# Optimization experiments

Hardware: AMD Instinct MI355X
Metric: run time of the kernel (lower is better)

## Reference

```python
import jax, jax.numpy as jnp
import numpy as np

N = 20000; P = 3; L_LP = 10; L_NS = 20; D = 128; OUT = 2; E = 640000; V_LP = 5000; V_NS = 10000


def _gru(x, lengths, W_ih, W_hh, b_ih, b_hh):
    # x: [B, T, Din]; returns last valid hidden state per sequence (pack_padded semantics)
    T = x.shape[1]
    xp = jnp.einsum('btd,gd->btg', x, W_ih) + b_ih  # [B, T, 3H]
    h0 = jnp.zeros((x.shape[0], W_hh.shape[1]), x.dtype)

    def step(h, inp):
        xpt, t = inp
        hp = h @ W_hh.T + b_hh
        xr, xz, xn = jnp.split(xpt, 3, axis=-1)
        hr, hz, hn = jnp.split(hp, 3, axis=-1)
        r = jax.nn.sigmoid(xr + hr)
        z = jax.nn.sigmoid(xz + hz)
        nn_ = jnp.tanh(xn + r * hn)
        h_new = (1.0 - z) * nn_ + z * h
        h = jnp.where((t < lengths)[:, None], h_new, h)
        return h, None

    hT, _ = jax.lax.scan(step, h0, (jnp.swapaxes(xp, 0, 1), jnp.arange(T)))
    return hT


def _gcn(x, src, dst, w, W, b, n):
    # PyG GCNConv: add self-loops (weight 1), symmetric normalization by in-degree
    loops = jnp.arange(n)
    s = jnp.concatenate([src, loops])
    d = jnp.concatenate([dst, loops])
    ww = jnp.concatenate([w, jnp.ones((n,), w.dtype)])
    deg = jax.ops.segment_sum(ww, d, num_segments=n)
    dinv = jnp.where(deg > 0, 1.0 / jnp.sqrt(deg), 0.0)
    norm = dinv[s] * ww * dinv[d]
    xw = x @ W.T
    return jax.ops.segment_sum(norm[:, None] * xw[s], d, num_segments=n) + b


def _lnorm(x, g, b):
    m = jnp.mean(x, axis=-1, keepdims=True)
    v = jnp.var(x, axis=-1, keepdims=True)
    return (x - m) / jnp.sqrt(v + 1e-5) * g + b


def _forward(x_ref, x_def, x_pdt, edge_weight, lp_emb, ns_emb, lp_Wih, lp_Whh, lp_bih, lp_bhh, ns_Wih, ns_Whh, ns_bih, ns_bhh, lp_fc_W, lp_fc_b, all_fc_W, all_fc_b, conv1_W, conv1_b, conv2_W, conv2_b, conv3_W, conv3_b, ln1_g, ln1_b, ln2_g, ln2_b, mp1_W, mp1_b, mp2_W, mp2_b, idx_lp, x_lp_length, idx_ns, x_ns_length, edge_index):
    n = idx_ns.shape[0]
    # long-path GRU encodings, one GRU run per path slot (vmapped over P)
    xl = lp_emb[idx_lp]  # [N, P, L_LP, D]
    gru_lp = lambda seq, lens: _gru(seq, lens, lp_Wih, lp_Whh, lp_bih, lp_bhh)
    h_lp = jax.vmap(gru_lp, in_axes=(1, 1))(xl, x_lp_length)  # [P, N, D]
    # torch.cat(h_list).view(N, D*P): row-major reshape of [P, N, D]
    x_lp = h_lp.reshape(n, P * D) @ lp_fc_W.T + lp_fc_b
    # natural-sequence GRU encoding
    x_ns = _gru(ns_emb[idx_ns], x_ns_length, ns_Wih, ns_Whh, ns_bih, ns_bhh)  # [N, D]
    # torch.cat(dim=0).view(N, 5D): faithful row-major reshape of [5N, D]
    x = jnp.concatenate([x_pdt, x_ref, x_def, x_lp, x_ns], axis=0).reshape(n, 5 * D)
    x = x @ all_fc_W.T + all_fc_b
    src, dst = edge_index[0], edge_index[1]
    convs = [(conv1_W, conv1_b), (conv2_W, conv2_b), (conv3_W, conv3_b)]
    lns = [(ln1_g, ln1_b), (ln2_g, ln2_b)]
    emb = x
    for i in range(3):
        x = _gcn(x, src, dst, edge_weight, convs[i][0], convs[i][1], n)
        emb = x
        x = jax.nn.relu(x)
        # dropout p=0.25 omitted (eval mode)
        if i < 2:
            x = _lnorm(x, lns[i][0], lns[i][1])
    x = x @ mp1_W.T + mp1_b
    x = x @ mp2_W.T + mp2_b
    return emb, jax.nn.log_softmax(x, axis=1)


def setup_inputs() -> dict:
    ks = jax.random.split(jax.random.key(0), 40)
    f32 = jnp.float32
    nrm = lambda k, sh, s: jax.random.normal(k, sh, f32) * s
    inp = {}
    inp['idx_lp'] = jax.random.randint(ks[0], (N, P, L_LP), 0, V_LP)
    inp['x_lp_length'] = jax.random.randint(ks[1], (N, P), 1, L_LP + 1)
    inp['idx_ns'] = jax.random.randint(ks[2], (N, L_NS), 0, V_NS)
    inp['x_ns_length'] = jax.random.randint(ks[3], (N,), 1, L_NS + 1)
    inp['x_ref'] = nrm(ks[4], (N, D), 1.0)
    inp['x_def'] = nrm(ks[5], (N, D), 1.0)
    inp['x_pdt'] = nrm(ks[6], (N, D), 1.0)
    inp['edge_index'] = jax.random.randint(ks[7], (2, E), 0, N)
    inp['edge_weight'] = jax.random.uniform(ks[8], (E,), f32)
    inp['lp_emb'] = nrm(ks[9], (V_LP, D), 0.5)
    inp['ns_emb'] = nrm(ks[10], (V_NS, D), 0.5)
    s = 0.08
    inp['lp_Wih'] = nrm(ks[11], (3 * D, D), s)
    inp['lp_Whh'] = nrm(ks[12], (3 * D, D), s)
    inp['lp_bih'] = nrm(ks[13], (3 * D,), s)
    inp['lp_bhh'] = nrm(ks[14], (3 * D,), s)
    inp['ns_Wih'] = nrm(ks[15], (3 * D, D), s)
    inp['ns_Whh'] = nrm(ks[16], (3 * D, D), s)
    inp['ns_bih'] = nrm(ks[17], (3 * D,), s)
    inp['ns_bhh'] = nrm(ks[18], (3 * D,), s)
    inp['lp_fc_W'] = nrm(ks[19], (D, P * D), 0.05)
    inp['lp_fc_b'] = nrm(ks[20], (D,), 0.05)
    inp['all_fc_W'] = nrm(ks[21], (D, 5 * D), 0.05)
    inp['all_fc_b'] = nrm(ks[22], (D,), 0.05)
    inp['conv1_W'] = nrm(ks[23], (D, D), 0.08)
    inp['conv1_b'] = nrm(ks[24], (D,), 0.05)
    inp['conv2_W'] = nrm(ks[25], (D, D), 0.08)
    inp['conv2_b'] = nrm(ks[26], (D,), 0.05)
    inp['conv3_W'] = nrm(ks[27], (D, D), 0.08)
    inp['conv3_b'] = nrm(ks[28], (D,), 0.05)
    inp['ln1_g'] = jnp.ones((D,), f32)
    inp['ln1_b'] = jnp.zeros((D,), f32)
    inp['ln2_g'] = jnp.ones((D,), f32)
    inp['ln2_b'] = jnp.zeros((D,), f32)
    inp['mp1_W'] = nrm(ks[29], (D, D), 0.08)
    inp['mp1_b'] = nrm(ks[30], (D,), 0.05)
    inp['mp2_W'] = nrm(ks[31], (OUT, D), 0.08)
    inp['mp2_b'] = nrm(ks[32], (OUT,), 0.05)
    return inp


def reference(idx_lp, x_lp_length, idx_ns, x_ns_length, x_ref, x_def, x_pdt, edge_index, edge_weight, lp_emb, ns_emb, lp_Wih, lp_Whh, lp_bih, lp_bhh, ns_Wih, ns_Whh, ns_bih, ns_bhh, lp_fc_W, lp_fc_b, all_fc_W, all_fc_b, conv1_W, conv1_b, conv2_W, conv2_b, conv3_W, conv3_b, ln1_g, ln1_b, ln2_g, ln2_b, mp1_W, mp1_b, mp2_W, mp2_b):
    return _forward(x_ref, x_def, x_pdt, edge_weight, lp_emb, ns_emb, lp_Wih, lp_Whh, lp_bih, lp_bhh, ns_Wih, ns_Whh, ns_bih, ns_bhh, lp_fc_W, lp_fc_b, all_fc_W, all_fc_b, conv1_W, conv1_b, conv2_W, conv2_b, conv3_W, conv3_b, ln1_g, ln1_b, ln2_g, ln2_b, mp1_W, mp1_b, mp2_W, mp2_b, idx_lp, x_lp_length, idx_ns, x_ns_length, edge_index)
```

## Files before the change

### kernel.cpp

```cpp
#include <hip/hip_runtime.h>
#include <math.h>

typedef unsigned short u16;
typedef short bf16x4 __attribute__((ext_vector_type(4)));
typedef short bf16x8 __attribute__((ext_vector_type(8)));
typedef float f32x16 __attribute__((ext_vector_type(16)));

#define NN 20000
#define PP 3
#define TLP 10
#define TNS 20
#define DD 128
#define EE 640000

__device__ __forceinline__ float bf2f(u16 u) {
  union { unsigned u; float f; } v; v.u = ((unsigned)u) << 16; return v.f;
}
__device__ __forceinline__ u16 f2bf(float f) {
  union { float f; unsigned u; } v; v.f = f;
  unsigned r = v.u + 0x7fffu + ((v.u >> 16) & 1u);
  return (u16)(r >> 16);
}
__device__ __forceinline__ short f2bf_hw(float f) {
  __bf16 b = (__bf16)f;
  return (short)__builtin_bit_cast(unsigned short, b);
}
__device__ __forceinline__ float loadf(const void* p, size_t i, int isf) {
  return isf ? ((const float*)p)[i] : bf2f(((const u16*)p)[i]);
}
__device__ __forceinline__ float fex2(float x) { return __builtin_amdgcn_exp2f(x); }
__device__ __forceinline__ float frcp(float x) { return __builtin_amdgcn_rcpf(x); }
__device__ __forceinline__ unsigned cvtpk(float lo, float hi) {
  unsigned r; asm("v_cvt_pk_bf16_f32 %0, %1, %2" : "=v"(r) : "v"(lo), "v"(hi));
  return r;
}

__global__ void k_detect(const void* probe, int* flag, int* bins,
                         int* __restrict__ counts) {
  if (blockIdx.x > 0) {
    int i = (blockIdx.x - 1) * 256 + threadIdx.x;
    if (i < NN) counts[i] = 0;
    return;
  }
  __shared__ int any;
  if (threadIdx.x == 0) any = 0;
  __syncthreads();
  if (threadIdx.x < 128) bins[threadIdx.x] = 0;
  const u16* p = (const u16*)probe;
  int bad = 0;
  for (int i = threadIdx.x; i < 4096; i += 256) {
    int e = (p[2 * i] >> 7) & 0xFF;
    if (e >= 0x9F) bad = 1;
  }
  if (bad) atomicOr(&any, 1);
  __syncthreads();
  if (threadIdx.x == 0) flag[0] = any;
}

struct CvtJobs {
  const void* src[16];
  int off[16];
  int n[16];
};

struct CvtJobsB {
  const void* src[12];
  int off[12];
  int n[12];
  int thr[12];
  float scA[12];
  float scB[12];
};

__global__ void k_megacvt(CvtJobsB j, CvtJobs jf, u16* __restrict__ dst,
                          float* __restrict__ fdst,
                          const int* __restrict__ lensLP,
                          const int* __restrict__ lensNS,
                          int* __restrict__ bins,
                          const int* __restrict__ e_dst,
                          int* __restrict__ counts,
                          const void* __restrict__ w2raw,
                          const void* __restrict__ b1raw,
                          const void* __restrict__ b2raw,
                          const void* __restrict__ mp1raw,
                          float* __restrict__ Wc, const int* flag) {
  const int isf = flag[0];
  const int B_CVT = 12 * 64;
  const int B_F = B_CVT + 16;
  const int LEN_B = (PP * NN + 255) / 256;
  const int B_LEN = B_F + LEN_B;
  const int HIST_B = (EE + 255) / 256;
  const int B_HIST = B_LEN + HIST_B;
  const int bx = (int)blockIdx.x;
  const int tid = threadIdx.x;
  if (bx < B_CVT) {
    const int job = bx >> 6;
    if (job < 2 && !isf) return;
    const int chunk = bx & 63;
    const void* s = j.src[job];
    u16* d = dst + j.off[job];
    const int n = j.n[job];
    const int thr = j.thr[job];
    const float sA = j.scA[job], sB = j.scB[job];
    for (int i = chunk * 256 + tid; i < n; i += 64 * 256)
      d[i] = f2bf(loadf(s, i, isf) * (i < thr ? sA : sB));
    return;
  }
  if (bx < B_F) {
    const int job = bx - B_CVT;
    const void* s = jf.src[job];
    float* d = fdst + jf.off[job];
    const int n = jf.n[job];
    for (int i = tid; i < n; i += 256) d[i] = loadf(s, i, isf);
    return;
  }
  if (bx < B_LEN) {
    int sg = (bx - B_F) * 256 + tid;
    int lane = tid & 63;
    int binL = 0, binN = 0;
    if (sg < PP * NN) binL = lensLP[(sg % NN) * PP + sg / NN];
    if (sg < NN) binN = lensNS[sg];
    for (int b = 1; b <= TLP; ++b) {
      unsigned long long m = __ballot(binL == b);
      if (m) {
        int leader = (int)(__ffsll((long long)m) - 1);
        if (lane == leader) atomicAdd(&bins[b], (int)__popcll(m));
      }
    }
    for (int b = 1; b <= TNS; ++b) {
      unsigned long long m = __ballot(binN == b);
      if (m) {
        int leader = (int)(__ffsll((long long)m) - 1);
        if (lane == leader) atomicAdd(&bins[64 + b], (int)__popcll(m));
      }
    }
    return;
  }
  if (bx < B_HIST) {
    int e = (bx - B_LEN) * 256 + tid;
    if (e < EE) atomicAdd(&counts[e_dst[e]], 1);
    return;
  }
  const int o = tid >> 7, k = tid & 127;
  float acc = 0.f;
  for (int d2 = 0; d2 < 128; ++d2)
    acc += loadf(w2raw, o * 128 + d2, isf) * loadf(mp1raw, (size_t)d2 * 128 + k, isf);
  Wc[tid] = acc;
  if (tid < 2) {
    float bacc = loadf(b2raw, tid, isf);
    for (int d2 = 0; d2 < 128; ++d2)
      bacc += loadf(w2raw, tid * 128 + d2, isf) * loadf(b1raw, d2, isf);
    Wc[256 + tid] = bacc;
  }
}

__global__ void k_lenfillboth(const int* __restrict__ lensLP,
                              const int* __restrict__ lensNS,
                              int* __restrict__ bins,
                              int* __restrict__ permLP,
                              int* __restrict__ permNS) {
  int sg = blockIdx.x * 256 + threadIdx.x;
  int lane = threadIdx.x & 63;
  int binL = 0, binN = 0;
  if (sg < PP * NN) binL = lensLP[(sg % NN) * PP + sg / NN];
  if (sg < NN) binN = lensNS[sg];
  int baseL = 0;
  for (int b = 1; b <= TLP; ++b) {
    unsigned long long m = __ballot(binL == b);
    if (m) {
      int leader = (int)(__ffsll((long long)m) - 1);
      int base = 0;
      if (lane == leader) base = atomicAdd(&bins[32 + b], (int)__popcll(m));
      base = __shfl(base, leader);
      if (binL == b) {
        int rank = (int)__popcll(m & ((1ull << lane) - 1ull));
        permLP[baseL + base + rank] = sg;
      }
    }
    baseL += bins[b];
  }
  int baseN = 0;
  for (int b = 1; b <= TNS; ++b) {
    unsigned long long m = __ballot(binN == b);
    if (m) {
      int leader = (int)(__ffsll((long long)m) - 1);
      int base = 0;
      if (lane == leader) base = atomicAdd(&bins[96 + b], (int)__popcll(m));
      base = __shfl(base, leader);
      if (binN == b) {
        int rank = (int)__popcll(m & ((1ull << lane) - 1ull));
        permNS[baseN + base + rank] = sg;
      }
    }
    baseN += bins[64 + b];
  }
}

__global__ __launch_bounds__(512, 2) void k_gru5(
    const int* __restrict__ permLP, const int* __restrict__ permNS, int nbNS,
    const u16* __restrict__ embLPc, const u16* __restrict__ embNSc,
    const u16* __restrict__ embLPr, const u16* __restrict__ embNSr,
    const int* __restrict__ idxLP, const int* __restrict__ idxNS,
    const int* __restrict__ lenLP, const int* __restrict__ lenNS,
    const u16* __restrict__ WihLP, const u16* __restrict__ WhhLP,
    const u16* __restrict__ WihNS, const u16* __restrict__ WhhNS,
    const float* __restrict__ bihLP, const float* __restrict__ bhhLP,
    const float* __restrict__ bihNS, const float* __restrict__ bhhNS,
    u16* __restrict__ HoutLP, u16* __restrict__ HoutNS, int nbLP,
    const int* __restrict__ counts, int* __restrict__ startA,
    int* __restrict__ cursorE, const int* __restrict__ flag) {
  __shared__ u16 xp[2][3][128][36];
  __shared__ u16 Hbf2[2][32][132];
  __shared__ int ivs[TNS][32];
  __shared__ int rowv[32], outv[32], lenv_s[32];
  __shared__ int Tbs;

  const int tid = threadIdx.x;
  if (blockIdx.x == 0) {
    int* part = (int*)ivs;
    const int C = (NN + 255) / 256;
    if (tid < 256) {
      int base = tid * C;
      int s = 0;
      for (int k = 0; k < C; ++k) {
        int i2 = base + k;
        s += (i2 < NN) ? counts[i2] : 0;
      }
      part[tid] = s;
    }
    __syncthreads();
    if (tid == 0) {
      int acc = 0;
      for (int k = 0; k < 256; ++k) { int v = part[k]; part[k] = acc; acc += v; }
    }
    __syncthreads();
    if (tid < 256) {
      int run = part[tid];
      int base = tid * C;
      for (int k = 0; k < C; ++k) {
        int i2 = base + k;
        if (i2 < NN) {
          int c = counts[i2];
          startA[i2] = run;
          cursorE[i2] = run;
          run += c;
        }
      }
      if (tid == 255) startA[NN] = run;
    }
    return;
  }
  const int bid = blockIdx.x - 1;
  const int isf = flag[0];
  const int isNS = bid < nbNS;
  const int chunk = isNS ? (nbNS - 1 - bid) : (nbLP - 1 - (bid - nbNS));
  const int* perm = isNS ? (permNS + chunk * 32) : (permLP + chunk * 32);
  const u16* embbf = isNS ? (isf ? embNSc : embNSr) : (isf ? embLPc : embLPr);
  const int* idx = isNS ? idxNS : idxLP;
  const int* lens = isNS ? lenNS : lenLP;
  const u16* Wih = isNS ? WihNS : WihLP;
  const u16* Whh = isNS ? WhhNS : WhhLP;
  const float* bih = isNS ? bihNS : bihLP;
  const float* bhh = isNS ? bhhNS : bhhLP;
  u16* Hout = isNS ? HoutNS : HoutLP;
  const int T = isNS ? TNS : TLP;

  const int w = tid >> 6, lane = tid & 63;
  const int l31 = lane & 31, lh = lane >> 5;
  const int role = w >> 2;
  const int j = w & 3;
  const int d = 32 * j + l31;

  if (tid < 32) {
    int sg = perm[tid];
    int row = isNS ? sg : ((sg % NN) * PP + sg / NN);
    rowv[tid] = row;
    outv[tid] = sg;
    lenv_s[tid] = lens[row];
  }
  __syncthreads();
  if (tid == 0) {
    int m = 1;
    for (int k = 0; k < 32; ++k) m = max(m, lenv_s[k]);
    Tbs = m;
  }
  __syncthreads();
  const int Tb = Tbs;

  for (int z = tid; z < Tb * 32; z += 512) {
    int s = z & 31, t = z >> 5;
    ivs[t][s] = idx[(size_t)rowv[s] * T + t];
  }
  for (int z = tid; z < 2112; z += 512) ((unsigned*)Hbf2[0])[z] = 0u;

  bf16x8 wf[24];
  {
    const u16* Ws = role ? Whh : Wih;
#pragma unroll
    for (int g = 0; g < 3; ++g)
#pragma unroll
      for (int kb = 0; kb < 8; ++kb)
        wf[g * 8 + kb] =
            *(const bf16x8*)(Ws + (size_t)(128 * g + d) * 128 + kb * 16 + lh * 8);
  }
  const float SA = -1.44269504088896f;
  const float SN = -2.88539008177793f;
  float ib0, ib1, ib2;
  if (!role) {
    ib0 = SA * (bih[d] + bhh[d]);
    ib1 = SA * (bih[128 + d] + bhh[128 + d]);
    ib2 = SN * bih[256 + d];
  } else {
    ib0 = 0.f;
    ib1 = 0.f;
    ib2 = SN * bhh[256 + d];
  }

  __syncthreads();
  int lenr[16];
#pragma unroll
  for (int rg = 0; rg < 16; ++rg)
    lenr[rg] = lenv_s[(rg & 3) + 8 * (rg >> 2) + 4 * lh];

  float h[16];
#pragma unroll
  for (int rg = 0; rg < 16; ++rg) h[rg] = 0.f;

  for (int i = 0; i <= Tb; ++i) {
    if (!role) {
      if (i < Tb) {
        bf16x8 Xf[8];
        const u16* erow = embbf + (size_t)ivs[i][l31] * 128 + lh * 8;
#pragma unroll
        for (int kb = 0; kb < 8; ++kb) Xf[kb] = *(const bf16x8*)(erow + kb * 16);
        f32x16 a0 = (f32x16)(ib0), a1 = (f32x16)(ib1), a2 = (f32x16)(ib2);
#pragma unroll
        for (int kb = 0; kb < 8; ++kb) {
          a0 = __builtin_amdgcn_mfma_f32_32x32x16_bf16(Xf[kb], wf[kb], a0, 0, 0, 0);
          a1 = __builtin_amdgcn_mfma_f32_32x32x16_bf16(Xf[kb], wf[8 + kb], a1, 0, 0, 0);
          a2 = __builtin_amdgcn_mfma_f32_32x32x16_bf16(Xf[kb], wf[16 + kb], a2, 0, 0, 0);
        }
        const int sl = i & 1;
#pragma unroll
        for (int rq = 0; rq < 4; ++rq) {
          int mo = 8 * rq + 4 * lh;
          bf16x4 p0, p1, p2;
#pragma unroll
          for (int q = 0; q < 4; ++q) {
            p0[q] = f2bf_hw(a0[4 * rq + q]);
            p1[q] = f2bf_hw(a1[4 * rq + q]);
            p2[q] = f2bf_hw(a2[4 * rq + q]);
          }
          *(bf16x4*)(&xp[sl][0][d][mo]) = p0;
          *(bf16x4*)(&xp[sl][1][d][mo]) = p1;
          *(bf16x4*)(&xp[sl][2][d][mo]) = p2;
        }
      }
    } else {
      if (i >= 1) {
        const int rs = (i - 1) & 1, wsl = i & 1;
        bf16x8 Hf[8];
#pragma unroll
        for (int kb = 0; kb < 8; ++kb) {
          bf16x4 lo = *(const bf16x4*)(&Hbf2[rs][l31][16 * kb + 8 * lh]);
          bf16x4 hi = *(const bf16x4*)(&Hbf2[rs][l31][16 * kb + 8 * lh + 4]);
          Hf[kb] = __builtin_shufflevector(lo, hi, 0, 1, 2, 3, 4, 5, 6, 7);
        }
        f32x16 a0 = (f32x16)(ib0), a1 = (f32x16)(ib1), a2 = (f32x16)(ib2);
#pragma unroll
        for (int kb = 0; kb < 8; ++kb) {
          a0 = __builtin_amdgcn_mfma_f32_32x32x16_bf16(Hf[kb], wf[kb], a0, 0, 0, 0);
          a1 = __builtin_amdgcn_mfma_f32_32x32x16_bf16(Hf[kb], wf[8 + kb], a1, 0, 0, 0);
          a2 = __builtin_amdgcn_mfma_f32_32x32x16_bf16(Hf[kb], wf[16 + kb], a2, 0, 0, 0);
        }
        const int t = i - 1;
#pragma unroll
        for (int rq = 0; rq < 4; ++rq) {
          int mo = 8 * rq + 4 * lh;
          bf16x4 x0 = *(const bf16x4*)(&xp[rs][0][d][mo]);
          bf16x4 x1 = *(const bf16x4*)(&xp[rs][1][d][mo]);
          bf16x4 x2 = *(const bf16x4*)(&xp[rs][2][d][mo]);
          float hq[4];
#pragma unroll
          for (int q = 0; q < 4; ++q) {
            int rg = 4 * rq + q;
            float r = frcp(1.f + fex2(a0[rg] + bf2f((u16)x0[q])));
            float z = frcp(1.f + fex2(a1[rg] + bf2f((u16)x1[q])));
            float s = fmaf(r, a2[rg], bf2f((u16)x2[q]));
            float nn_ = fmaf(2.f, frcp(1.f + fex2(s)), -1.f);
            float hnew = fmaf(z, h[rg] - nn_, nn_);
            h[rg] = (t < lenr[rg]) ? hnew : h[rg];
            hq[q] = h[rg];
          }
          unsigned pa = cvtpk(hq[0], hq[1]);
          unsigned pb = cvtpk(hq[2], hq[3]);
          Hbf2[wsl][mo + 0][d] = (u16)pa;
          Hbf2[wsl][mo + 1][d] = (u16)(pa >> 16);
          Hbf2[wsl][mo + 2][d] = (u16)pb;
          Hbf2[wsl][mo + 3][d] = (u16)(pb >> 16);
        }
      }
    }
    __syncthreads();
  }

  if (role) {
#pragma unroll
    for (int rg = 0; rg < 16; ++rg) {
      int m = (rg & 3) + 8 * (rg >> 2) + 4 * lh;
      Hout[(size_t)outv[m] * 128 + d] = f2bf(h[rg]);
    }
  }
}

__global__ __launch_bounds__(128) void k_gemm_mfma(
    const void* __restrict__ A0, const void* __restrict__ A1,
    const void* __restrict__ A2, const u16* __restrict__ A3,
    const u16* __restrict__ A4, int mode, int K,
    const u16* __restrict__ W, const float* __restrict__ bias,
    void* __restrict__ Cout, int out_bf, int M, const int* __restrict__ flag,
    const int* __restrict__ esrc, const int* __restrict__ edst,
    const void* __restrict__ ew, int* __restrict__ cursor,
    int2* __restrict__ csr, const int* __restrict__ startT,
    float* __restrict__ dinvOut, int tailN, int tailMode, int gemmBlocks) {
  const int isf = flag[0];
  const int tid = threadIdx.x;
  if ((int)blockIdx.x >= gemmBlocks) {
    int i = ((int)blockIdx.x - gemmBlocks) * 128 + tid;
    if (i < tailN) {
      if (tailMode == 1) {
        int s = esrc[i];
        float wv = loadf(ew, i, isf);
        int p = atomicAdd(&cursor[edst[i]], 1);
        csr[p] = make_int2(s, __float_as_int(wv));
      } else {
        int a = startT[i], b = startT[i + 1];
        float sum = 1.f;
        for (int k = a; k < b; ++k) sum += __int_as_float(csr[k].y);
        dinvOut[i] = 1.f / sqrtf(sum);
      }
    }
    return;
  }
  const int w = tid >> 6, lane = tid & 63;
  const int l31 = lane & 31, lh = lane >> 5;
  const int w23 = w;
  const int mbase = blockIdx.x * 32;
  const int row = mbase + l31;
  const int rowc = row < M ? row : M - 1;

  f32x16 acc0 = (f32x16)(0.f), acc1 = (f32x16)(0.f);
  const int nk = K >> 4;
  for (int kb = 0; kb < nk; ++kb) {
    bf16x8 a;
    if (mode == 0) {
      a = *(const bf16x8*)((const u16*)A0 + (size_t)rowc * K + kb * 16 + lh * 8);
    } else {
      int r5 = 5 * rowc + (kb >> 3);
      int slot = r5 / NN;
      int inner = r5 - slot * NN;
      int koff = (kb & 7) * 16 + lh * 8;
      if (slot < 3) {
        const void* p = (slot == 0) ? A0 : (slot == 1) ? A1 : A2;
        if (isf) {
          const float* fp = (const float*)p + (size_t)inner * 128 + koff;
          float4 v0 = *(const float4*)fp;
          float4 v1 = *(const float4*)(fp + 4);
          a[0] = (short)f2bf(v0.x); a[1] = (short)f2bf(v0.y);
          a[2] = (short)f2bf(v0.z); a[3] = (short)f2bf(v0.w);
          a[4] = (short)f2bf(v1.x); a[5] = (short)f2bf(v1.y);
          a[6] = (short)f2bf(v1.z); a[7] = (short)f2bf(v1.w);
        } else {
          a = *(const bf16x8*)((const u16*)p + (size_t)inner * 128 + koff);
        }
      } else {
        const u16* p = (slot == 3) ? A3 : A4;
        a = *(const bf16x8*)(p + (size_t)inner * 128 + koff);
      }
    }
    const u16* wp = W + (size_t)(64 * w23 + l31) * K + kb * 16 + lh * 8;
    bf16x8 b0 = *(const bf16x8*)wp;
    bf16x8 b1 = *(const bf16x8*)(wp + (size_t)32 * K);
    acc0 = __builtin_amdgcn_mfma_f32_32x32x16_bf16(a, b0, acc0, 0, 0, 0);
    acc1 = __builtin_amdgcn_mfma_f32_32x32x16_bf16(a, b1, acc1, 0, 0, 0);
  }
  const int col0 = 64 * w23 + l31;
  const float bv0 = bias ? bias[col0] : 0.f;
  const float bv1 = bias ? bias[col0 + 32] : 0.f;
#pragma unroll
  for (int rg = 0; rg < 16; ++rg) {
    int m = (rg & 3) + 8 * (rg >> 2) + 4 * lh;
    int grow = mbase + m;
    if (grow < M) {
      float v0 = acc0[rg] + bv0, v1 = acc1[rg] + bv1;
      if (out_bf) {
        ((u16*)Cout)[(size_t)grow * 128 + col0] = f2bf(v0);
        ((u16*)Cout)[(size_t)grow * 128 + col0 + 32] = f2bf(v1);
      } else {
        ((float*)Cout)[(size_t)grow * 128 + col0] = v0;
        ((float*)Cout)[(size_t)grow * 128 + col0 + 32] = v1;
      }
    }
  }
}

__global__ __launch_bounds__(256) void k_gcn_gather(
    const int* __restrict__ start, const int2* __restrict__ csr,
    const float* __restrict__ dinv, const u16* __restrict__ xwbf,
    const float* __restrict__ bias, const float* __restrict__ g,
    const float* __restrict__ b, u16* __restrict__ out_bf,
    void* __restrict__ dout, const float* __restrict__ Wc,
    const int* __restrict__ flag, int mode) {
  int v = blockIdx.x * 4 + (threadIdx.x >> 6);
  int lane = threadIdx.x & 63;
  if (v >= NN) return;
  const int c0 = 2 * lane;
  float acc0 = 0.f, acc1 = 0.f;
  int i = start[v];
  const int i1 = start[v + 1];
  for (; i + 4 <= i1; i += 4) {
    int2 e0 = csr[i], e1 = csr[i + 1], e2 = csr[i + 2], e3 = csr[i + 3];
    unsigned p0 = *(const unsigned*)(xwbf + (size_t)e0.x * 128 + c0);
    unsigned p1 = *(const unsigned*)(xwbf + (size_t)e1.x * 128 + c0);
    unsigned p2 = *(const unsigned*)(xwbf + (size_t)e2.x * 128 + c0);
    unsigned p3 = *(const unsigned*)(xwbf + (size_t)e3.x * 128 + c0);
    float f0 = __int_as_float(e0.y) * dinv[e0.x];
    float f1 = __int_as_float(e1.y) * dinv[e1.x];
    float f2 = __int_as_float(e2.y) * dinv[e2.x];
    float f3 = __int_as_float(e3.y) * dinv[e3.x];
    acc0 += f0 * bf2f((u16)(p0 & 0xffff)) + f1 * bf2f((u16)(p1 & 0xffff)) +
            f2 * bf2f((u16)(p2 & 0xffff)) + f3 * bf2f((u16)(p3 & 0xffff));
    acc1 += f0 * bf2f((u16)(p0 >> 16)) + f1 * bf2f((u16)(p1 >> 16)) +
            f2 * bf2f((u16)(p2 >> 16)) + f3 * bf2f((u16)(p3 >> 16));
  }
  if (i + 2 <= i1) {
    int2 e0 = csr[i], e1 = csr[i + 1];
    unsigned p0 = *(const unsigned*)(xwbf + (size_t)e0.x * 128 + c0);
    unsigned p1 = *(const unsigned*)(xwbf + (size_t)e1.x * 128 + c0);
    float f0 = __int_as_float(e0.y) * dinv[e0.x];
    float f1 = __int_as_float(e1.y) * dinv[e1.x];
    acc0 += f0 * bf2f((u16)(p0 & 0xffff)) + f1 * bf2f((u16)(p1 & 0xffff));
    acc1 += f0 * bf2f((u16)(p0 >> 16)) + f1 * bf2f((u16)(p1 >> 16));
    i += 2;
  }
  if (i < i1) {
    int2 e = csr[i];
    float c = __int_as_float(e.y) * dinv[e.x];
    unsigned pv = *(const unsigned*)(xwbf + (size_t)e.x * 128 + c0);
    acc0 += c * bf2f((u16)(pv & 0xffff));
    acc1 += c * bf2f((u16)(pv >> 16));
  }
  float dv = dinv[v];
  unsigned sv = *(const unsigned*)(xwbf + (size_t)v * 128 + c0);
  float y0 = bias[c0] + dv * (dv * bf2f((u16)(sv & 0xffff)) + acc0);
  float y1 = bias[c0 + 1] + dv * (dv * bf2f((u16)(sv >> 16)) + acc1);
  if (mode == 1) {
    if (flag[0]) {
      *(float2*)((float*)dout + (size_t)v * 128 + c0) = make_float2(y0, y1);
    } else {
      unsigned pk = (unsigned)f2bf(y0) | ((unsigned)f2bf(y1) << 16);
      *(unsigned*)((u16*)dout + (size_t)v * 128 + c0) = pk;
    }
    float x0 = fmaxf(y0, 0.f), x1 = fmaxf(y1, 0.f);
    float p0 = x0 * Wc[c0] + x1 * Wc[c0 + 1];
    float p1 = x0 * Wc[128 + c0] + x1 * Wc[128 + c0 + 1];
#pragma unroll
    for (int off = 32; off; off >>= 1) {
      p0 += __shfl_xor(p0, off);
      p1 += __shfl_xor(p1, off);
    }
    if (lane == 0) {
      float v0 = p0 + Wc[256], v1 = p1 + Wc[257];
      float m = fmaxf(v0, v1);
      float ls = m + logf(__expf(v0 - m) + __expf(v1 - m));
      size_t base = (size_t)NN * 128 + (size_t)v * 2;
      if (flag[0]) {
        ((float*)dout)[base + 0] = v0 - ls;
        ((float*)dout)[base + 1] = v1 - ls;
      } else {
        unsigned pk = (unsigned)f2bf(v0 - ls) | ((unsigned)f2bf(v1 - ls) << 16);
        *(unsigned*)((u16*)dout + base) = pk;
      }
    }
  } else {
    float x0 = fmaxf(y0, 0.f), x1 = fmaxf(y1, 0.f);
    float s_ = x0 + x1;
#pragma unroll
    for (int off = 32; off; off >>= 1) s_ += __shfl_xor(s_, off);
    float mean = s_ * (1.f / 128.f);
    float e0 = x0 - mean, e1 = x1 - mean;
    float vv = e0 * e0 + e1 * e1;
#pragma unroll
    for (int off = 32; off; off >>= 1) vv += __shfl_xor(vv, off);
    float inv = 1.f / sqrtf(vv * (1.f / 128.f) + 1e-5f);
    unsigned pk = (unsigned)f2bf(e0 * inv * g[c0] + b[c0]) |
                  ((unsigned)f2bf(e1 * inv * g[c0 + 1] + b[c0 + 1]) << 16);
    *(unsigned*)(out_bf + (size_t)v * 128 + c0) = pk;
  }
}

extern "C" void kernel_launch(void* const* d_in, const int* in_sizes, int n_in,
                              void* d_out, int out_size, void* d_ws, size_t ws_size,
                              hipStream_t stream) {
  const int* idx_lp = (const int*)d_in[0];
  const int* len_lp = (const int*)d_in[1];
  const int* idx_ns = (const int*)d_in[2];
  const int* len_ns = (const int*)d_in[3];
  const void* x_ref = d_in[4];
  const void* x_def = d_in[5];
  const void* x_pdt = d_in[6];
  const int* eidx   = (const int*)d_in[7];
  const void* ew    = d_in[8];
  const void* lp_emb = d_in[9];
  const void* ns_emb = d_in[10];

  char* cur = (char*)d_ws;
  auto alloc = [&](size_t bytes, size_t align) -> void* {
    size_t a = ((size_t)cur + align - 1) & ~(align - 1);
    cur = (char*)(a + bytes);
    return (void*)a;
  };
  int* flag     = (int*)alloc(64, 64);
  float* smallW = (float*)alloc(3104 * 4, 16);
  float* f_Wc   = (float*)alloc(260 * 4, 16);
  float* f_dinv = (float*)alloc(NN * 4, 16);
  int* counts   = (int*)alloc(NN * 4, 16);
  int* startA   = (int*)alloc((NN + 1) * 4, 16);
  int* cursorE  = (int*)alloc(NN * 4, 16);
  int* bins     = (int*)alloc(128 * 4, 16);
  int* perm_lp  = (int*)alloc(PP * NN * 4, 16);
  int* perm_ns  = (int*)alloc(NN * 4, 16);
  int2* csr2    = (int2*)alloc((size_t)EE * 8, 16);
  u16* ub       = (u16*)alloc((size_t)20233216 * 2, 16);
  u16* embbf_lp = ub;
  u16* embbf_ns = ub + 640000;
  u16* wg_lpih  = ub + 1920000;
  u16* wg_lphh  = ub + 1969152;
  u16* wg_nsih  = ub + 2018304;
  u16* wg_nshh  = ub + 2067456;
  u16* wg_lpfc  = ub + 2116608;
  u16* wg_allfc = ub + 2165760;
  u16* wg_c1    = ub + 2247680;
  u16* wg_c2    = ub + 2264064;
  u16* wg_c3    = ub + 2280448;
  u16* hbf_lp   = ub + 2313216;
  u16* hbf_ns   = ub + 9993216;
  u16* lp_bf    = ub + 12553216;
  u16* xcur_bf  = ub + 15113216;
  u16* xw_bf    = ub + 17673216;

  static const int fn[16] = {384, 384, 384, 384, 128, 128, 128, 128,
                             128, 128, 128, 128, 128, 128, 256, 2};
  static const int fsrc[16] = {13, 14, 17, 18, 20, 22, 24, 26,
                               28, 29, 30, 31, 32, 34, 35, 36};
  CvtJobs jf;
  int foff[16];
  {
    int off = 0;
    for (int j = 0; j < 16; ++j) {
      jf.src[j] = d_in[fsrc[j]];
      jf.off[j] = off;
      jf.n[j] = fn[j];
      foff[j] = off;
      off += fn[j];
    }
  }
  float* b_lpbih = smallW + foff[0];
  float* b_lpbhh = smallW + foff[1];
  float* b_nsbih = smallW + foff[2];
  float* b_nsbhh = smallW + foff[3];
  float* b_lpfc  = smallW + foff[4];
  float* b_allfc = smallW + foff[5];
  float* b_conv[3] = {smallW + foff[6], smallW + foff[7], smallW + foff[8]};
  float* g_ln[2] = {smallW + foff[9], smallW + foff[11]};
  float* b_ln[2] = {smallW + foff[10], smallW + foff[12]};

  static const int bn[12] = {640000, 1280000, 49152, 49152, 49152, 49152,
                             49152, 81920, 16384, 16384, 16384, 0};
  static const int bsrc[12] = {9, 10, 11, 12, 15, 16, 19, 21, 23, 25, 27, 33};
  static const int boff[12] = {0, 640000, 1920000, 1969152, 2018304, 2067456,
                               2116608, 2165760, 2247680, 2264064, 2280448,
                               2296832};
  CvtJobsB jb;
  for (int j = 0; j < 12; ++j) {
    jb.src[j] = d_in[bsrc[j]];
    jb.off[j] = boff[j];
    jb.n[j] = bn[j];
    const bool gw = (j >= 2 && j <= 5);
    jb.thr[j] = gw ? 32768 : 0;
    jb.scA[j] = gw ? -1.44269504088896f : 1.f;
    jb.scB[j] = gw ? -2.88539008177793f : 1.f;
  }

  const int* e_src = eidx;
  const int* e_dst = eidx + EE;

  const int initBlocks = (NN + 255) / 256;
  k_detect<<<1 + initBlocks, 256, 0, stream>>>(lp_emb, flag, bins, counts);

  const int lenBlocks = (PP * NN + 255) / 256;
  const int histBlocks = (EE + 255) / 256;
  k_megacvt<<<12 * 64 + 16 + lenBlocks + histBlocks + 1, 256, 0, stream>>>(
      jb, jf, ub, smallW, len_lp, len_ns, bins, e_dst, counts,
      d_in[35], d_in[34], d_in[36], d_in[33], f_Wc, flag);

  k_lenfillboth<<<lenBlocks, 256, 0, stream>>>(len_lp, len_ns, bins,
                                               perm_lp, perm_ns);

  const int nbLP = PP * NN / 32, nbNS = NN / 32;
  k_gru5<<<1 + nbLP + nbNS, 512, 0, stream>>>(
      perm_lp, perm_ns, nbNS, embbf_lp, embbf_ns,
      (const u16*)lp_emb, (const u16*)ns_emb,
      idx_lp, idx_ns, len_lp, len_ns,
      wg_lpih, wg_lphh, wg_nsih, wg_nshh, b_lpbih, b_lpbhh, b_nsbih, b_nsbhh,
      hbf_lp, hbf_ns, nbLP, counts, startA, cursorE, flag);

  const int gg = (NN + 31) / 32;
  const int fillBlocks = (EE + 127) / 128;
  const int degBlocks = (NN + 127) / 128;
  k_gemm_mfma<<<gg + fillBlocks, 128, 0, stream>>>(
      hbf_lp, nullptr, nullptr, nullptr, nullptr, 0, 384, wg_lpfc, b_lpfc,
      lp_bf, 1, NN, flag, e_src, e_dst, ew, cursorE, csr2, nullptr, nullptr,
      EE, 1, gg);
  k_gemm_mfma<<<gg + degBlocks, 128, 0, stream>>>(
      x_pdt, x_ref, x_def, lp_bf, hbf_ns, 1, 640, wg_allfc, b_allfc,
      xcur_bf, 1, NN, flag, nullptr, nullptr, nullptr, nullptr, csr2, startA,
      f_dinv, NN, 2, gg);

  const u16* wgc[3] = {wg_c1, wg_c2, wg_c3};
  for (int l = 0; l < 3; ++l) {
    k_gemm_mfma<<<gg, 128, 0, stream>>>(
        xcur_bf, nullptr, nullptr, nullptr, nullptr, 0, DD, wgc[l], nullptr,
        xw_bf, 1, NN, flag, nullptr, nullptr, nullptr, nullptr, nullptr,
        nullptr, nullptr, 0, 0, gg);
    if (l < 2) {
      k_gcn_gather<<<NN / 4, 256, 0, stream>>>(startA, csr2, f_dinv, xw_bf,
                                               b_conv[l], g_ln[l], b_ln[l],
                                               xcur_bf, nullptr, nullptr,
                                               flag, 0);
    } else {
      k_gcn_gather<<<NN / 4, 256, 0, stream>>>(startA, csr2, f_dinv, xw_bf,
                                               b_conv[l], nullptr, nullptr,
                                               nullptr, d_out, f_Wc,
                                               flag, 1);
    }
  }
}
```

Baseline: 823.0 us.

## Fuse all-fc GEMM with conv1 linear and GCN gather+LN with next conv GEMM

The all-fc GEMM now feeds its 32-row output tile through shared memory directly into the conv1 weight GEMM. Each GCN aggregation plus ReLU and LayerNorm now computes the next layer's X·W in the same block via MFMA. This removes three standalone GEMM launches and the round-trips of intermediate activations through global memory. The cost is larger blocks with serialized gather-then-GEMM phases, where half the waves sit idle during the MFMA step.

```diff
diff --git a/kernel.cpp b/kernel.cpp
--- a/kernel.cpp
+++ b/kernel.cpp
@@ -504,13 +504,185 @@
   }
 }
 
+__global__ __launch_bounds__(128) void k_allfc_g1(
+    const void* __restrict__ A0, const void* __restrict__ A1,
+    const void* __restrict__ A2, const u16* __restrict__ A3,
+    const u16* __restrict__ A4,
+    const u16* __restrict__ W, const float* __restrict__ bias,
+    const u16* __restrict__ W1, u16* __restrict__ xwOut,
+    const int* __restrict__ flag,
+    const int2* __restrict__ csr, const int* __restrict__ startT,
+    float* __restrict__ dinvOut, int gemmBlocks) {
+  __shared__ u16 ylds[32][136];
+  const int isf = flag[0];
+  const int tid = threadIdx.x;
+  if ((int)blockIdx.x >= gemmBlocks) {
+    int i = ((int)blockIdx.x - gemmBlocks) * 128 + tid;
+    if (i < NN) {
+      int a = startT[i], b = startT[i + 1];
+      float sum = 1.f;
+      for (int k = a; k < b; ++k) sum += __int_as_float(csr[k].y);
+      dinvOut[i] = 1.f / sqrtf(sum);
+    }
+    return;
+  }
+  const int w = tid >> 6, lane = tid & 63;
+  const int l31 = lane & 31, lh = lane >> 5;
+  const int w23 = w;
+  const int mbase = blockIdx.x * 32;
+  const int rowc = mbase + l31;
+
+  f32x16 acc0 = (f32x16)(0.f), acc1 = (f32x16)(0.f);
+  const int K = 640;
+  for (int kb = 0; kb < (K >> 4); ++kb) {
+    bf16x8 a;
+    {
+      int r5 = 5 * rowc + (kb >> 3);
+      int slot = r5 / NN;
+      int inner = r5 - slot * NN;
+      int koff = (kb & 7) * 16 + lh * 8;
+      if (slot < 3) {
+        const void* p = (slot == 0) ? A0 : (slot == 1) ? A1 : A2;
+        if (isf) {
+          const float* fp = (const float*)p + (size_t)inner * 128 + koff;
+          float4 v0 = *(const float4*)fp;
+          float4 v1 = *(const float4*)(fp + 4);
+          a[0] = (short)f2bf(v0.x); a[1] = (short)f2bf(v0.y);
+          a[2] = (short)f2bf(v0.z); a[3] = (short)f2bf(v0.w);
+          a[4] = (short)f2bf(v1.x); a[5] = (short)f2bf(v1.y);
+          a[6] = (short)f2bf(v1.z); a[7] = (short)f2bf(v1.w);
+        } else {
+          a = *(const bf16x8*)((const u16*)p + (size_t)inner * 128 + koff);
+        }
+      } else {
+        const u16* p = (slot == 3) ? A3 : A4;
+        a = *(const bf16x8*)(p + (size_t)inner * 128 + koff);
+      }
+    }
+    const u16* wp = W + (size_t)(64 * w23 + l31) * K + kb * 16 + lh * 8;
+    bf16x8 b0 = *(const bf16x8*)wp;
+    bf16x8 b1 = *(const bf16x8*)(wp + (size_t)32 * K);
+    acc0 = __builtin_amdgcn_mfma_f32_32x32x16_bf16(a, b0, acc0, 0, 0, 0);
+    acc1 = __builtin_amdgcn_mfma_f32_32x32x16_bf16(a, b1, acc1, 0, 0, 0);
+  }
+  const int col0 = 64 * w23 + l31;
+  const float bv0 = bias[col0], bv1 = bias[col0 + 32];
+#pragma unroll
+  for (int rg = 0; rg < 16; ++rg) {
+    int m = (rg & 3) + 8 * (rg >> 2) + 4 * lh;
+    ylds[m][col0] = f2bf(acc0[rg] + bv0);
+    ylds[m][col0 + 32] = f2bf(acc1[rg] + bv1);
+  }
+  __syncthreads();
+  f32x16 c0a = (f32x16)(0.f), c1a = (f32x16)(0.f);
+#pragma unroll
+  for (int kb = 0; kb < 8; ++kb) {
+    bf16x8 a = *(const bf16x8*)(&ylds[l31][kb * 16 + lh * 8]);
+    const u16* wp = W1 + (size_t)(64 * w23 + l31) * 128 + kb * 16 + lh * 8;
+    bf16x8 b0 = *(const bf16x8*)wp;
+    bf16x8 b1 = *(const bf16x8*)(wp + (size_t)32 * 128);
+    c0a = __builtin_amdgcn_mfma_f32_32x32x16_bf16(a, b0, c0a, 0, 0, 0);
+    c1a = __builtin_amdgcn_mfma_f32_32x32x16_bf16(a, b1, c1a, 0, 0, 0);
+  }
+#pragma unroll
+  for (int rg = 0; rg < 16; ++rg) {
+    int m = (rg & 3) + 8 * (rg >> 2) + 4 * lh;
+    xwOut[(size_t)(mbase + m) * 128 + col0] = f2bf(c0a[rg]);
+    xwOut[(size_t)(mbase + m) * 128 + col0 + 32] = f2bf(c1a[rg]);
+  }
+}
+
+__global__ __launch_bounds__(512) void k_gcnfused(
+    const int* __restrict__ start, const int2* __restrict__ csr,
+    const float* __restrict__ dinv, const u16* __restrict__ xwIn,
+    const float* __restrict__ bias, const float* __restrict__ g,
+    const float* __restrict__ b, const u16* __restrict__ Wn,
+    u16* __restrict__ xwOut) {
+  __shared__ u16 ylds[32][136];
+  const int tid = threadIdx.x;
+  const int wv = tid >> 6, lane = tid & 63;
+  const int vbase = blockIdx.x * 32;
+  const int c0 = 2 * lane;
+  for (int s = 0; s < 4; ++s) {
+    const int r = wv * 4 + s;
+    const int v = vbase + r;
+    float acc0 = 0.f, acc1 = 0.f;
+    int i = start[v];
+    const int i1 = start[v + 1];
+    for (; i + 4 <= i1; i += 4) {
+      int2 e0 = csr[i], e1 = csr[i + 1], e2 = csr[i + 2], e3 = csr[i + 3];
+      unsigned p0 = *(const unsigned*)(xwIn + (size_t)e0.x * 128 + c0);
+      unsigned p1 = *(const unsigned*)(xwIn + (size_t)e1.x * 128 + c0);
+      unsigned p2 = *(const unsigned*)(xwIn + (size_t)e2.x * 128 + c0);
+      unsigned p3 = *(const unsigned*)(xwIn + (size_t)e3.x * 128 + c0);
+      float f0 = __int_as_float(e0.y) * dinv[e0.x];
+      float f1 = __int_as_float(e1.y) * dinv[e1.x];
+      float f2 = __int_as_float(e2.y) * dinv[e2.x];
+      float f3 = __int_as_float(e3.y) * dinv[e3.x];
+      acc0 += f0 * bf2f((u16)(p0 & 0xffff)) + f1 * bf2f((u16)(p1 & 0xffff)) +
+              f2 * bf2f((u16)(p2 & 0xffff)) + f3 * bf2f((u16)(p3 & 0xffff));
+      acc1 += f0 * bf2f((u16)(p0 >> 16)) + f1 * bf2f((u16)(p1 >> 16)) +
+              f2 * bf2f((u16)(p2 >> 16)) + f3 * bf2f((u16)(p3 >> 16));
+    }
+    if (i + 2 <= i1) {
+      int2 e0 = csr[i], e1 = csr[i + 1];
+      unsigned p0 = *(const unsigned*)(xwIn + (size_t)e0.x * 128 + c0);
+      unsigned p1 = *(const unsigned*)(xwIn + (size_t)e1.x * 128 + c0);
+      float f0 = __int_as_float(e0.y) * dinv[e0.x];
+      float f1 = __int_as_float(e1.y) * dinv[e1.x];
+      acc0 += f0 * bf2f((u16)(p0 & 0xffff)) + f1 * bf2f((u16)(p1 & 0xffff));
+      acc1 += f0 * bf2f((u16)(p0 >> 16)) + f1 * bf2f((u16)(p1 >> 16));
+      i += 2;
+    }
+    if (i < i1) {
+      int2 e = csr[i];
+      float c = __int_as_float(e.y) * dinv[e.x];
+      unsigned pv = *(const unsigned*)(xwIn + (size_t)e.x * 128 + c0);
+      acc0 += c * bf2f((u16)(pv & 0xffff));
+      acc1 += c * bf2f((u16)(pv >> 16));
+    }
+    float dv = dinv[v];
+    unsigned sv = *(const unsigned*)(xwIn + (size_t)v * 128 + c0);
+    float y0 = bias[c0] + dv * (dv * bf2f((u16)(sv & 0xffff)) + acc0);
+    float y1 = bias[c0 + 1] + dv * (dv * bf2f((u16)(sv >> 16)) + acc1);
+    float x0 = fmaxf(y0, 0.f), x1 = fmaxf(y1, 0.f);
+    float s_ = x0 + x1;
+#pragma unroll
+    for (int off = 32; off; off >>= 1) s_ += __shfl_xor(s_, off);
+    float mean = s_ * (1.f / 128.f);
+    float e0 = x0 - mean, e1 = x1 - mean;
+    float vv = e0 * e0 + e1 * e1;
+#pragma unroll
+    for (int off = 32; off; off >>= 1) vv += __shfl_xor(vv, off);
+    float inv = 1.f / sqrtf(vv * (1.f / 128.f) + 1e-5f);
+    unsigned pk = (unsigned)f2bf(e0 * inv * g[c0] + b[c0]) |
+                  ((unsigned)f2bf(e1 * inv * g[c0 + 1] + b[c0 + 1]) << 16);
+    *(unsigned*)(&ylds[r][c0]) = pk;
+  }
+  __syncthreads();
+  if (wv >= 4) return;
+  const int l31 = lane & 31, lh = lane >> 5;
+  f32x16 acc = (f32x16)(0.f);
+#pragma unroll
+  for (int kb = 0; kb < 8; ++kb) {
+    bf16x8 a = *(const bf16x8*)(&ylds[l31][kb * 16 + lh * 8]);
+    bf16x8 b0 = *(const bf16x8*)(Wn + (size_t)(32 * wv + l31) * 128 + kb * 16 + lh * 8);
+    acc = __builtin_amdgcn_mfma_f32_32x32x16_bf16(a, b0, acc, 0, 0, 0);
+  }
+  const int col0 = 32 * wv + l31;
+#pragma unroll
+  for (int rg = 0; rg < 16; ++rg) {
+    int m = (rg & 3) + 8 * (rg >> 2) + 4 * lh;
+    xwOut[(size_t)(vbase + m) * 128 + col0] = f2bf(acc[rg]);
+  }
+}
+
 __global__ __launch_bounds__(256) void k_gcn_gather(
     const int* __restrict__ start, const int2* __restrict__ csr,
     const float* __restrict__ dinv, const u16* __restrict__ xwbf,
-    const float* __restrict__ bias, const float* __restrict__ g,
-    const float* __restrict__ b, u16* __restrict__ out_bf,
+    const float* __restrict__ bias,
     void* __restrict__ dout, const float* __restrict__ Wc,
-    const int* __restrict__ flag, int mode) {
+    const int* __restrict__ flag) {
   int v = blockIdx.x * 4 + (threadIdx.x >> 6);
   int lane = threadIdx.x & 63;
   if (v >= NN) return;
@@ -554,48 +726,32 @@
   unsigned sv = *(const unsigned*)(xwbf + (size_t)v * 128 + c0);
   float y0 = bias[c0] + dv * (dv * bf2f((u16)(sv & 0xffff)) + acc0);
   float y1 = bias[c0 + 1] + dv * (dv * bf2f((u16)(sv >> 16)) + acc1);
-  if (mode == 1) {
+  if (flag[0]) {
+    *(float2*)((float*)dout + (size_t)v * 128 + c0) = make_float2(y0, y1);
+  } else {
+    unsigned pk = (unsigned)f2bf(y0) | ((unsigned)f2bf(y1) << 16);
+    *(unsigned*)((u16*)dout + (size_t)v * 128 + c0) = pk;
+  }
+  float x0 = fmaxf(y0, 0.f), x1 = fmaxf(y1, 0.f);
+  float p0 = x0 * Wc[c0] + x1 * Wc[c0 + 1];
+  float p1 = x0 * Wc[128 + c0] + x1 * Wc[128 + c0 + 1];
+#pragma unroll
+  for (int off = 32; off; off >>= 1) {
+    p0 += __shfl_xor(p0, off);
+    p1 += __shfl_xor(p1, off);
+  }
+  if (lane == 0) {
+    float v0 = p0 + Wc[256], v1 = p1 + Wc[257];
+    float m = fmaxf(v0, v1);
+    float ls = m + logf(__expf(v0 - m) + __expf(v1 - m));
+    size_t base = (size_t)NN * 128 + (size_t)v * 2;
     if (flag[0]) {
-      *(float2*)((float*)dout + (size_t)v * 128 + c0) = make_float2(y0, y1);
+      ((float*)dout)[base + 0] = v0 - ls;
+      ((float*)dout)[base + 1] = v1 - ls;
     } else {
-      unsigned pk = (unsigned)f2bf(y0) | ((unsigned)f2bf(y1) << 16);
-      *(unsigned*)((u16*)dout + (size_t)v * 128 + c0) = pk;
-    }
-    float x0 = fmaxf(y0, 0.f), x1 = fmaxf(y1, 0.f);
-    float p0 = x0 * Wc[c0] + x1 * Wc[c0 + 1];
-    float p1 = x0 * Wc[128 + c0] + x1 * Wc[128 + c0 + 1];
-#pragma unroll
-    for (int off = 32; off; off >>= 1) {
-      p0 += __shfl_xor(p0, off);
-      p1 += __shfl_xor(p1, off);
-    }
-    if (lane == 0) {
-      float v0 = p0 + Wc[256], v1 = p1 + Wc[257];
-      float m = fmaxf(v0, v1);
-      float ls = m + logf(__expf(v0 - m) + __expf(v1 - m));
-      size_t base = (size_t)NN * 128 + (size_t)v * 2;
-      if (flag[0]) {
-        ((float*)dout)[base + 0] = v0 - ls;
-        ((float*)dout)[base + 1] = v1 - ls;
-      } else {
-        unsigned pk = (unsigned)f2bf(v0 - ls) | ((unsigned)f2bf(v1 - ls) << 16);
-        *(unsigned*)((u16*)dout + base) = pk;
-      }
-    }
-  } else {
-    float x0 = fmaxf(y0, 0.f), x1 = fmaxf(y1, 0.f);
-    float s_ = x0 + x1;
-#pragma unroll
-    for (int off = 32; off; off >>= 1) s_ += __shfl_xor(s_, off);
-    float mean = s_ * (1.f / 128.f);
-    float e0 = x0 - mean, e1 = x1 - mean;
-    float vv = e0 * e0 + e1 * e1;
-#pragma unroll
-    for (int off = 32; off; off >>= 1) vv += __shfl_xor(vv, off);
-    float inv = 1.f / sqrtf(vv * (1.f / 128.f) + 1e-5f);
-    unsigned pk = (unsigned)f2bf(e0 * inv * g[c0] + b[c0]) |
-                  ((unsigned)f2bf(e1 * inv * g[c0 + 1] + b[c0 + 1]) << 16);
-    *(unsigned*)(out_bf + (size_t)v * 128 + c0) = pk;
+      unsigned pk = (unsigned)f2bf(v0 - ls) | ((unsigned)f2bf(v1 - ls) << 16);
+      *(unsigned*)((u16*)dout + base) = pk;
+    }
   }
 }
 
@@ -646,8 +802,8 @@
   u16* hbf_lp   = ub + 2313216;
   u16* hbf_ns   = ub + 9993216;
   u16* lp_bf    = ub + 12553216;
-  u16* xcur_bf  = ub + 15113216;
-  u16* xw_bf    = ub + 17673216;
+  u16* xwA      = ub + 15113216;
+  u16* xwB      = ub + 17673216;
 
   static const int fn[16] = {384, 384, 384, 384, 128, 128, 128, 128,
                              128, 128, 128, 128, 128, 128, 256, 2};
@@ -722,27 +878,14 @@
       hbf_lp, nullptr, nullptr, nullptr, nullptr, 0, 384, wg_lpfc, b_lpfc,
       lp_bf, 1, NN, flag, e_src, e_dst, ew, cursorE, csr2, nullptr, nullptr,
       EE, 1, gg);
-  k_gemm_mfma<<<gg + degBlocks, 128, 0, stream>>>(
-      x_pdt, x_ref, x_def, lp_bf, hbf_ns, 1, 640, wg_allfc, b_allfc,
-      xcur_bf, 1, NN, flag, nullptr, nullptr, nullptr, nullptr, csr2, startA,
-      f_dinv, NN, 2, gg);
-
-  const u16* wgc[3] = {wg_c1, wg_c2, wg_c3};
-  for (int l = 0; l < 3; ++l) {
-    k_gemm_mfma<<<gg, 128, 0, stream>>>(
-        xcur_bf, nullptr, nullptr, nullptr, nullptr, 0, DD, wgc[l], nullptr,
-        xw_bf, 1, NN, flag, nullptr, nullptr, nullptr, nullptr, nullptr,
-        nullptr, nullptr, 0, 0, gg);
-    if (l < 2) {
-      k_gcn_gather<<<NN / 4, 256, 0, stream>>>(startA, csr2, f_dinv, xw_bf,
-                                               b_conv[l], g_ln[l], b_ln[l],
-                                               xcur_bf, nullptr, nullptr,
-                                               flag, 0);
-    } else {
-      k_gcn_gather<<<NN / 4, 256, 0, stream>>>(startA, csr2, f_dinv, xw_bf,
-                                               b_conv[l], nullptr, nullptr,
-                                               nullptr, d_out, f_Wc,
-                                               flag, 1);
-    }
-  }
-}
+  k_allfc_g1<<<gg + degBlocks, 128, 0, stream>>>(
+      x_pdt, x_ref, x_def, lp_bf, hbf_ns, wg_allfc, b_allfc, wg_c1, xwA,
+      flag, csr2, startA, f_dinv, gg);
+
+  k_gcnfused<<<gg, 512, 0, stream>>>(startA, csr2, f_dinv, xwA,
+                                     b_conv[0], g_ln[0], b_ln[0], wg_c2, xwB);
+  k_gcnfused<<<gg, 512, 0, stream>>>(startA, csr2, f_dinv, xwB,
+                                     b_conv[1], g_ln[1], b_ln[1], wg_c3, xwA);
+  k_gcn_gather<<<NN / 4, 256, 0, stream>>>(startA, csr2, f_dinv, xwA,
+                                           b_conv[2], d_out, f_Wc, flag);
+}
```

Result: faster. 799.7 us (-2.8%).
